# Performance work log

Hardware: AMD Instinct MI355X
Metric: run time of the kernel (lower is better)

## Reference

```python
import jax, jax.numpy as jnp
import numpy as np

E, S = 32768, 16
H, D_IN, EDGE_IN = 128, 128, 16
N_SRC, N_DST = 20000, 5000
HEADS, LAYERS, NUM_CLASS = 8, 2, 10
DH = H // HEADS


def _layer_norm(x, g, b, eps=1e-5):
    mu = jnp.mean(x, axis=-1, keepdims=True)
    var = jnp.mean((x - mu) ** 2, axis=-1, keepdims=True)
    return (x - mu) * jax.lax.rsqrt(var + eps) * g + b


def _encoder(e, e_mask, Wqkv, bqkv, Wo, bo, ln1_g, ln1_b, W1, b1, W2, b2, ln2_g, ln2_b):
    # e: [E,S,H]; e_mask: [E,S], True = padding. Post-norm encoder (PyTorch default).
    neg = jnp.float32(-1e9)
    for l in range(LAYERS):
        qkv = e @ Wqkv[l] + bqkv[l]                      # [E,S,3H]
        q, k, v = jnp.split(qkv, 3, axis=-1)
        q = q.reshape(E, S, HEADS, DH)
        k = k.reshape(E, S, HEADS, DH)
        v = v.reshape(E, S, HEADS, DH)
        scores = jnp.einsum('eqhd,ekhd->ehqk', q, k) / np.float32(np.sqrt(DH))
        scores = jnp.where(e_mask[:, None, None, :], neg, scores)
        attn = jax.nn.softmax(scores, axis=-1)
        ctx = jnp.einsum('ehqk,ekhd->eqhd', attn, v).reshape(E, S, H)
        e = _layer_norm(e + (ctx @ Wo[l] + bo[l]), ln1_g[l], ln1_b[l])
        ff = jax.nn.relu(e @ W1[l] + b1[l]) @ W2[l] + b2[l]
        e = _layer_norm(e + ff, ln2_g[l], ln2_b[l])
    return e


def _forward(node_features, edge_features, seq_times, subg_norm,
             W_ein, b_ein, enc_Wqkv, enc_bqkv, enc_Wo, enc_bo, enc_ln1_g, enc_ln1_b,
             enc_W1, enc_b1, enc_W2, enc_b2, enc_ln2_g, enc_ln2_b,
             W_eout, b_eout, W_node, b_node, W_fc, b_fc,
             e_len, e_mask, src_ids, dst_ids, layer_nid):
    h = node_features                                             # [N_src, D_IN]
    self_h = h[layer_nid]                                         # [N_dst, D_IN]
    self_h_tmp = jnp.concatenate([self_h, jnp.zeros((N_DST, H), h.dtype)], axis=1) @ W_eout + b_eout
    # message_func: per-edge sequence -> embed -> transformer -> pool -> concat with src h
    e = jnp.concatenate([edge_features, seq_times[..., None]], axis=-1)  # [E,S,EDGE_IN]
    e = jax.nn.relu(e @ W_ein + b_ein)                                   # [E,S,H]
    e = _encoder(e, e_mask, enc_Wqkv, enc_bqkv, enc_Wo, enc_bo,
                 enc_ln1_g, enc_ln1_b, enc_W1, enc_b1, enc_W2, enc_b2, enc_ln2_g, enc_ln2_b)
    valid = (~e_mask).astype(e.dtype)[..., None]
    e = jnp.sum(e * valid, axis=1) / e_len.astype(e.dtype)[:, None]      # masked mean pool [E,H]
    m = jax.nn.relu(jnp.concatenate([h[src_ids], e], axis=1) @ W_eout + b_eout)  # [E,H]
    h_agg = jax.ops.segment_sum(m, dst_ids, num_segments=N_DST)          # ragged mailbox sum
    hh = (h_agg - self_h_tmp) * subg_norm                                # NodeUpdate (train branch)
    z = jax.nn.relu(jnp.concatenate([self_h, hh], axis=1) @ W_node + b_node)
    return z @ W_fc + b_fc                                               # [N_dst, NUM_CLASS]


def setup_inputs() -> dict:
    key = jax.random.key(0)
    ks = jax.random.split(key, 32)
    inp = {}
    inp['node_features'] = jax.random.normal(ks[0], (N_SRC, D_IN), jnp.float32)
    inp['edge_features'] = jax.random.normal(ks[1], (E, S, EDGE_IN - 1), jnp.float32)
    inp['seq_times'] = jax.random.uniform(ks[2], (E, S), jnp.float32)
    e_len = jax.random.randint(ks[3], (E,), 1, S + 1).astype(jnp.int32)
    inp['e_len'] = e_len
    inp['e_mask'] = jnp.arange(S, dtype=jnp.int32)[None, :] >= e_len[:, None]  # True = pad
    inp['src_ids'] = jax.random.randint(ks[4], (E,), 0, N_SRC).astype(jnp.int32)
    inp['dst_ids'] = jax.random.randint(ks[5], (E,), 0, N_DST).astype(jnp.int32)
    inp['layer_nid'] = jax.random.randint(ks[6], (N_DST,), 0, N_SRC).astype(jnp.int32)
    inp['subg_norm'] = jax.random.uniform(ks[7], (N_DST, 1), jnp.float32, minval=0.01, maxval=1.0)

    def lin(k, fi, fo):
        return jax.random.normal(k, (fi, fo), jnp.float32) / np.float32(np.sqrt(fi))

    inp['W_ein'] = lin(ks[8], EDGE_IN, H); inp['b_ein'] = jnp.zeros((H,), jnp.float32)
    inp['enc_Wqkv'] = jax.random.normal(ks[9], (LAYERS, H, 3 * H), jnp.float32) / np.float32(np.sqrt(H))
    inp['enc_bqkv'] = jnp.zeros((LAYERS, 3 * H), jnp.float32)
    inp['enc_Wo'] = jax.random.normal(ks[10], (LAYERS, H, H), jnp.float32) / np.float32(np.sqrt(H))
    inp['enc_bo'] = jnp.zeros((LAYERS, H), jnp.float32)
    inp['enc_ln1_g'] = jnp.ones((LAYERS, H), jnp.float32); inp['enc_ln1_b'] = jnp.zeros((LAYERS, H), jnp.float32)
    inp['enc_W1'] = jax.random.normal(ks[11], (LAYERS, H, H), jnp.float32) / np.float32(np.sqrt(H))
    inp['enc_b1'] = jnp.zeros((LAYERS, H), jnp.float32)
    inp['enc_W2'] = jax.random.normal(ks[12], (LAYERS, H, H), jnp.float32) / np.float32(np.sqrt(H))
    inp['enc_b2'] = jnp.zeros((LAYERS, H), jnp.float32)
    inp['enc_ln2_g'] = jnp.ones((LAYERS, H), jnp.float32); inp['enc_ln2_b'] = jnp.zeros((LAYERS, H), jnp.float32)
    inp['W_eout'] = lin(ks[13], D_IN + H, H); inp['b_eout'] = jnp.zeros((H,), jnp.float32)
    inp['W_node'] = lin(ks[14], D_IN + H, H); inp['b_node'] = jnp.zeros((H,), jnp.float32)
    inp['W_fc'] = lin(ks[15], H, NUM_CLASS); inp['b_fc'] = jnp.zeros((NUM_CLASS,), jnp.float32)
    return inp


def reference(node_features, edge_features, seq_times, e_len, e_mask, src_ids, dst_ids,
              layer_nid, subg_norm, W_ein, b_ein, enc_Wqkv, enc_bqkv, enc_Wo, enc_bo,
              enc_ln1_g, enc_ln1_b, enc_W1, enc_b1, enc_W2, enc_b2, enc_ln2_g, enc_ln2_b,
              W_eout, b_eout, W_node, b_node, W_fc, b_fc):
    return _forward(node_features, edge_features, seq_times, subg_norm,
                    W_ein, b_ein, enc_Wqkv, enc_bqkv, enc_Wo, enc_bo, enc_ln1_g, enc_ln1_b,
                    enc_W1, enc_b1, enc_W2, enc_b2, enc_ln2_g, enc_ln2_b,
                    W_eout, b_eout, W_node, b_node, W_fc, b_fc,
                    e_len, e_mask, src_ids, dst_ids, layer_nid)
```

## Files before the change

### kernel.cpp

```cpp
#include <hip/hip_runtime.h>
#include <hip/hip_bf16.h>

typedef __attribute__((ext_vector_type(8))) short bf16x8;
typedef __attribute__((ext_vector_type(4))) short s16x4;
typedef __attribute__((ext_vector_type(4))) float f32x4;

#define E_N      32768
#define N_DST_N  5000
#define NCLS     10

#define OFF_HAGG   0
#define OFF_POOL   2560000
#define OFF_WPACK  10948608

#define PK_QKV(l)  ((l) * 6144)
#define PK_WO(l)   (12288 + (l) * 2048)
#define PK_W1(l)   (16384 + (l) * 2048)
#define PK_W2(l)   (20480 + (l) * 2048)
#define PK_WEOUT   24576
#define PK_WEIN    28672

__device__ __forceinline__ unsigned short f2bf(float f) {
    __hip_bfloat16 h = __float2bfloat16(f);
    unsigned short u;
    __builtin_memcpy(&u, &h, 2);
    return u;
}
__device__ __forceinline__ unsigned int f2bf2(float lo, float hi) {
    __hip_bfloat162 h = __float22bfloat162_rn(make_float2(lo, hi));
    unsigned int u;
    __builtin_memcpy(&u, &h, 4);
    return u;
}

__global__ void pack_weights(const float* __restrict__ Wqkv,
                             const float* __restrict__ Wo,
                             const float* __restrict__ W1,
                             const float* __restrict__ W2,
                             const float* __restrict__ W_eout,
                             const float* __restrict__ W_ein,
                             unsigned short* __restrict__ wpack) {
    int gid = blockIdx.x * 256 + threadIdx.x;
    if (gid >= 233472) return;
    if (gid >= 229376) {
        int li = gid - 229376;
        int j = li & 7, lane = (li >> 3) & 63, t = li >> 9;
        int k = ((lane >> 4) << 3) + j;
        int n = t * 16 + (lane & 15);
        wpack[gid] = (k < 16) ? f2bf(W_ein[k * 128 + n]) : (unsigned short)0;
        return;
    }
    int id = gid;
    const float* src; int K, N, li;
    if (id < 98304)       { src = Wqkv + (id / 49152) * 49152; li = id % 49152; K = 128; N = 384; }
    else if (id < 131072) { id -= 98304;  src = Wo + (id / 16384) * 16384; li = id % 16384; K = 128; N = 128; }
    else if (id < 163840) { id -= 131072; src = W1 + (id / 16384) * 16384; li = id % 16384; K = 128; N = 128; }
    else if (id < 196608) { id -= 163840; src = W2 + (id / 16384) * 16384; li = id % 16384; K = 128; N = 128; }
    else                  { li = id - 196608; src = W_eout; K = 256; N = 128; }
    int j = li & 7, lane = (li >> 3) & 63, rest = li >> 9;
    int ks = K >> 5;
    int kk = rest % ks, t = rest / ks;
    int k = kk * 32 + ((lane >> 4) << 3) + j;
    int n = t * 16 + (lane & 15);
    wpack[gid] = f2bf(src[k * N + n]);
}

__device__ __forceinline__ void layer_norm_reg(
    float res[2][2][4],
    const float gcol[2], const float bcol[2],
    unsigned short (*a_bf)[136],
    float (*psum)[4], float (*psq)[4],
    int w, int c16, int row4)
{
    float sv[2][4], qv[2][4];
#pragma unroll
    for (int rt = 0; rt < 2; ++rt)
#pragma unroll
        for (int r = 0; r < 4; ++r) {
            float x0 = res[rt][0][r], x1 = res[rt][1][r];
            float s = x0 + x1;
            float q = x0 * x0 + x1 * x1;
#pragma unroll
            for (int d = 1; d < 16; d <<= 1) {
                s += __shfl_xor(s, d);
                q += __shfl_xor(q, d);
            }
            sv[rt][r] = s; qv[rt][r] = q;
        }
    if (c16 == 0) {
#pragma unroll
        for (int rt = 0; rt < 2; ++rt)
#pragma unroll
            for (int r = 0; r < 4; ++r) {
                int row = rt * 16 + row4 + r;
                psum[row][w] = sv[rt][r];
                psq[row][w]  = qv[rt][r];
            }
    }
    __syncthreads();
#pragma unroll
    for (int rt = 0; rt < 2; ++rt)
#pragma unroll
        for (int r = 0; r < 4; ++r) {
            int row = rt * 16 + row4 + r;
            float4 S = *(const float4*)&psum[row][0];
            float4 Q = *(const float4*)&psq[row][0];
            float sum = (S.x + S.y) + (S.z + S.w);
            float sq  = (Q.x + Q.y) + (Q.z + Q.w);
            float mu  = sum * (1.f / 128.f);
            float var = sq * (1.f / 128.f) - mu * mu;
            float inv = rsqrtf(var + 1e-5f);
#pragma unroll
            for (int ti = 0; ti < 2; ++ti) {
                float y = (res[rt][ti][r] - mu) * inv * gcol[ti] + bcol[ti];
                res[rt][ti][r] = y;
                a_bf[row][w * 32 + ti * 16 + c16] = f2bf(y);
            }
        }
}

__global__ __launch_bounds__(256) void edge_kernel(
    const float* __restrict__ edge_features,
    const float* __restrict__ seq_times,
    const int*   __restrict__ e_len,
    const float* __restrict__ b_ein,
    const float* __restrict__ bqkv,  const float* __restrict__ bo,
    const float* __restrict__ ln1_g, const float* __restrict__ ln1_b,
    const float* __restrict__ b1,    const float* __restrict__ b2,
    const float* __restrict__ ln2_g, const float* __restrict__ ln2_b,
    const unsigned short* __restrict__ wpack,
    unsigned short* __restrict__ pooled)
{
    __shared__ __align__(16) unsigned short a_bf[32][136];
    __shared__ __align__(16) unsigned short q_bf[32][136];
    __shared__ __align__(16) unsigned short k_bf[32][136];
    __shared__ __align__(16) union VX {
        unsigned short vT[2][128][24];
        unsigned short x_bf[32][40];
    } vx;
    __shared__ __align__(16) float psum[32][4];
    __shared__ __align__(16) float psq[32][4];

    const int tid  = threadIdx.x;
    const int e0   = blockIdx.x * 2;
    const int lane = tid & 63;
    const int w    = tid >> 6;
    const int c16  = lane & 15;
    const int g    = lane >> 4;
    const int row4 = g << 2;
    const int kblk = g << 3;
    const int len0 = e_len[e0];
    const int len1 = e_len[e0 + 1];
    const f32x4 z4 = {0.f, 0.f, 0.f, 0.f};

    float res[2][2][4];

    float lnG[2][2][2], lnB[2][2][2];
#pragma unroll
    for (int l = 0; l < 2; ++l)
#pragma unroll
        for (int ti = 0; ti < 2; ++ti) {
            int col = w * 32 + ti * 16 + c16;
            lnG[l][0][ti] = ln1_g[l * 128 + col];
            lnB[l][0][ti] = ln1_b[l * 128 + col];
            lnG[l][1][ti] = ln2_g[l * 128 + col];
            lnB[l][1][ti] = ln2_b[l * 128 + col];
        }

    for (int idx = tid; idx < 1024; idx += 256) {
        int r = idx >> 5, cc = idx & 31;
        int e = r >> 4, s = r & 15;
        float v = 0.f;
        if (cc < 15)       v = edge_features[(e0 + e) * 240 + s * 15 + cc];
        else if (cc == 15) v = seq_times[(e0 + e) * 16 + s];
        vx.x_bf[r][cc] = f2bf(v);
    }
    __syncthreads();

    const bf16x8* WP = (const bf16x8*)wpack;

    {
        bf16x8 axf[2];
#pragma unroll
        for (int rt = 0; rt < 2; ++rt)
            axf[rt] = *(const bf16x8*)&vx.x_bf[rt * 16 + c16][kblk];
#pragma unroll
        for (int ti = 0; ti < 2; ++ti) {
            bf16x8 bw = WP[PK_WEIN + (2 * w + ti) * 64 + lane];
            int col = (2 * w + ti) * 16 + c16;
            float bias = b_ein[col];
#pragma unroll
            for (int rt = 0; rt < 2; ++rt) {
                f32x4 acc = __builtin_amdgcn_mfma_f32_16x16x32_bf16(axf[rt], bw, z4, 0, 0, 0);
#pragma unroll
                for (int r = 0; r < 4; ++r) {
                    float v = fmaxf(acc[r] + bias, 0.f);
                    res[rt][ti][r] = v;
                    a_bf[rt * 16 + row4 + r][col] = f2bf(v);
                }
            }
        }
    }
    __syncthreads();

    for (int l = 0; l < 2; ++l) {
        {
            bf16x8 af[2][4];
#pragma unroll
            for (int rt = 0; rt < 2; ++rt)
#pragma unroll
                for (int kk = 0; kk < 4; ++kk)
                    af[rt][kk] = *(const bf16x8*)&a_bf[rt * 16 + c16][kk * 32 + kblk];
            const bf16x8* B = WP + PK_QKV(l);
#pragma unroll
            for (int seg = 0; seg < 3; ++seg) {
#pragma unroll
                for (int ti = 0; ti < 2; ++ti) {
                    bf16x8 bq[4];
#pragma unroll
                    for (int kk = 0; kk < 4; ++kk)
                        bq[kk] = B[((seg * 8 + 2 * w + ti) * 4 + kk) * 64 + lane];
                    int col = (2 * w + ti) * 16 + c16;
                    float bias = bqkv[l * 384 + seg * 128 + col];
#pragma unroll
                    for (int rt = 0; rt < 2; ++rt) {
                        f32x4 acc = z4;
#pragma unroll
                        for (int kk = 0; kk < 4; ++kk)
                            acc = __builtin_amdgcn_mfma_f32_16x16x32_bf16(
                                af[rt][kk], bq[kk], acc, 0, 0, 0);
                        if (seg == 0) {
#pragma unroll
                            for (int r = 0; r < 4; ++r)
                                q_bf[rt * 16 + row4 + r][col] = f2bf(acc[r] + bias);
                        } else if (seg == 1) {
#pragma unroll
                            for (int r = 0; r < 4; ++r)
                                k_bf[rt * 16 + row4 + r][col] = f2bf(acc[r] + bias);
                        } else {
                            union { unsigned int u[2]; s16x4 v; } pk;
                            pk.u[0] = f2bf2(acc[0] + bias, acc[1] + bias);
                            pk.u[1] = f2bf2(acc[2] + bias, acc[3] + bias);
                            *(s16x4*)&vx.vT[rt][col][row4] = pk.v;
                        }
                    }
                }
            }
        }
        __syncthreads();

#pragma unroll
        for (int i = 0; i < 4; ++i) {
            int pp = w * 4 + i;
            int e  = pp >> 3;
            int hb = (pp & 7) * 16;
            int er = e * 16;
            int len = e ? len1 : len0;
            bf16x8 kf = {0,0,0,0,0,0,0,0};
            bf16x8 qf = {0,0,0,0,0,0,0,0};
            bf16x8 vf = {0,0,0,0,0,0,0,0};
            if (lane < 32) {
                kf = *(const bf16x8*)&k_bf[er + c16][hb + kblk];
                qf = *(const bf16x8*)&q_bf[er + c16][hb + kblk];
                vf = *(const bf16x8*)&vx.vT[e][hb + c16][kblk];
            }
            f32x4 st = __builtin_amdgcn_mfma_f32_16x16x32_bf16(kf, qf, z4, 0, 0, 0);
            float sv[4]; float mx = -1e30f;
#pragma unroll
            for (int r = 0; r < 4; ++r) {
                sv[r] = st[r] * 0.25f;
                if (4 * g + r < len) mx = fmaxf(mx, sv[r]);
            }
            mx = fmaxf(mx, __shfl_xor(mx, 16));
            mx = fmaxf(mx, __shfl_xor(mx, 32));
            float p[4]; float sum = 0.f;
#pragma unroll
            for (int r = 0; r < 4; ++r) {
                float pe = (4 * g + r < len) ? __expf(sv[r] - mx) : 0.f;
                p[r] = pe; sum += pe;
            }
            sum += __shfl_xor(sum, 16);
            sum += __shfl_xor(sum, 32);
            float inv = __fdividef(1.f, sum);
            unsigned int own0 = f2bf2(p[0] * inv, p[1] * inv);
            unsigned int own1 = f2bf2(p[2] * inv, p[3] * inv);
            unsigned int t0a = (unsigned int)__shfl((int)own0, (lane + 16) & 63);
            unsigned int t1a = (unsigned int)__shfl((int)own1, (lane + 16) & 63);
            unsigned int t0b = (unsigned int)__shfl((int)own0, (lane + 32) & 63);
            unsigned int t1b = (unsigned int)__shfl((int)own1, (lane + 32) & 63);
            union { unsigned int u[4]; bf16x8 v; } pb;
            if (g == 0)      { pb.u[0] = own0; pb.u[1] = own1; pb.u[2] = t0a; pb.u[3] = t1a; }
            else if (g == 1) { pb.u[0] = t0a;  pb.u[1] = t1a;  pb.u[2] = t0b; pb.u[3] = t1b; }
            else             { pb.u[0] = 0; pb.u[1] = 0; pb.u[2] = 0; pb.u[3] = 0; }
            f32x4 ct = __builtin_amdgcn_mfma_f32_16x16x32_bf16(vf, pb.v, z4, 0, 0, 0);
            union { unsigned int u[2]; s16x4 v; } cpk;
            cpk.u[0] = f2bf2(ct[0], ct[1]);
            cpk.u[1] = f2bf2(ct[2], ct[3]);
            *(s16x4*)&a_bf[er + c16][hb + 4 * g] = cpk.v;
        }
        __syncthreads();

        {
            bf16x8 af[2][4];
#pragma unroll
            for (int rt = 0; rt < 2; ++rt)
#pragma unroll
                for (int kk = 0; kk < 4; ++kk)
                    af[rt][kk] = *(const bf16x8*)&a_bf[rt * 16 + c16][kk * 32 + kblk];
            const bf16x8* B = WP + PK_WO(l);
#pragma unroll
            for (int ti = 0; ti < 2; ++ti) {
                bf16x8 bw[4];
#pragma unroll
                for (int kk = 0; kk < 4; ++kk)
                    bw[kk] = B[((2 * w + ti) * 4 + kk) * 64 + lane];
                int col = (2 * w + ti) * 16 + c16;
                float bias = bo[l * 128 + col];
#pragma unroll
                for (int rt = 0; rt < 2; ++rt) {
                    f32x4 acc = z4;
#pragma unroll
                    for (int kk = 0; kk < 4; ++kk)
                        acc = __builtin_amdgcn_mfma_f32_16x16x32_bf16(
                            af[rt][kk], bw[kk], acc, 0, 0, 0);
#pragma unroll
                    for (int r = 0; r < 4; ++r)
                        res[rt][ti][r] += acc[r] + bias;
                }
            }
        }
        layer_norm_reg(res, lnG[l][0], lnB[l][0], a_bf, psum, psq, w, c16, row4);
        __syncthreads();

        {
            bf16x8 af[2][4];
#pragma unroll
            for (int rt = 0; rt < 2; ++rt)
#pragma unroll
                for (int kk = 0; kk < 4; ++kk)
                    af[rt][kk] = *(const bf16x8*)&a_bf[rt * 16 + c16][kk * 32 + kblk];
            const bf16x8* B = WP + PK_W1(l);
#pragma unroll
            for (int ti = 0; ti < 2; ++ti) {
                bf16x8 bw[4];
#pragma unroll
                for (int kk = 0; kk < 4; ++kk)
                    bw[kk] = B[((2 * w + ti) * 4 + kk) * 64 + lane];
                int col = (2 * w + ti) * 16 + c16;
                float bias = b1[l * 128 + col];
#pragma unroll
                for (int rt = 0; rt < 2; ++rt) {
                    f32x4 acc = z4;
#pragma unroll
                    for (int kk = 0; kk < 4; ++kk)
                        acc = __builtin_amdgcn_mfma_f32_16x16x32_bf16(
                            af[rt][kk], bw[kk], acc, 0, 0, 0);
#pragma unroll
                    for (int r = 0; r < 4; ++r)
                        q_bf[rt * 16 + row4 + r][col] =
                            f2bf(fmaxf(acc[r] + bias, 0.f));
                }
            }
        }
        __syncthreads();

        {
            bf16x8 af[2][4];
#pragma unroll
            for (int rt = 0; rt < 2; ++rt)
#pragma unroll
                for (int kk = 0; kk < 4; ++kk)
                    af[rt][kk] = *(const bf16x8*)&q_bf[rt * 16 + c16][kk * 32 + kblk];
            const bf16x8* B = WP + PK_W2(l);
#pragma unroll
            for (int ti = 0; ti < 2; ++ti) {
                bf16x8 bw[4];
#pragma unroll
                for (int kk = 0; kk < 4; ++kk)
                    bw[kk] = B[((2 * w + ti) * 4 + kk) * 64 + lane];
                int col = (2 * w + ti) * 16 + c16;
                float bias = b2[l * 128 + col];
#pragma unroll
                for (int rt = 0; rt < 2; ++rt) {
                    f32x4 acc = z4;
#pragma unroll
                    for (int kk = 0; kk < 4; ++kk)
                        acc = __builtin_amdgcn_mfma_f32_16x16x32_bf16(
                            af[rt][kk], bw[kk], acc, 0, 0, 0);
#pragma unroll
                    for (int r = 0; r < 4; ++r)
                        res[rt][ti][r] += acc[r] + bias;
                }
            }
        }
        layer_norm_reg(res, lnG[l][1], lnB[l][1], a_bf, psum, psq, w, c16, row4);
        __syncthreads();
    }

#pragma unroll
    for (int rt = 0; rt < 2; ++rt) {
        int len = rt ? len1 : len0;
        float fln = (float)len;
#pragma unroll
        for (int ti = 0; ti < 2; ++ti) {
            float s = 0.f;
#pragma unroll
            for (int r = 0; r < 4; ++r)
                if (row4 + r < len) s += res[rt][ti][r];
            s += __shfl_xor(s, 16);
            s += __shfl_xor(s, 32);
            if (lane < 16)
                pooled[(e0 + rt) * 128 + w * 32 + ti * 16 + c16] = f2bf(s / fln);
        }
    }
}

__global__ __launch_bounds__(256) void edge_out_kernel(
    const float* __restrict__ node_features,
    const int* __restrict__ src_ids, const int* __restrict__ dst_ids,
    const unsigned short* __restrict__ pooled,
    const unsigned short* __restrict__ wpack,
    const float* __restrict__ b_eout,
    float* __restrict__ h_agg)
{
    __shared__ __align__(16) unsigned short a2[16][264];
    __shared__ int dst_s[16];
    const int tid = threadIdx.x, lane = tid & 63, w = tid >> 6;
    const int e0 = blockIdx.x * 16;

    {
        int r = tid >> 4, cm = tid & 15;
        int e = e0 + r;
        int src = src_ids[e];
#pragma unroll
        for (int m = 0; m < 8; ++m) {
            int col = cm + 16 * m;
            a2[r][col] = f2bf(node_features[src * 128 + col]);
        }
#pragma unroll
        for (int m = 0; m < 8; ++m) {
            int col = cm + 16 * m;
            a2[r][128 + col] = pooled[e * 128 + col];
        }
        if (tid < 16) dst_s[tid] = dst_ids[e0 + tid];
    }
    __syncthreads();

    const int c16 = lane & 15, row4 = (lane >> 4) << 2, kblk = (lane >> 4) << 3;
    bf16x8 af[8];
#pragma unroll
    for (int kk = 0; kk < 8; ++kk)
        af[kk] = *(const bf16x8*)&a2[c16][kk * 32 + kblk];
    const bf16x8* B = (const bf16x8*)wpack + PK_WEOUT;
#pragma unroll
    for (int ti = 0; ti < 2; ++ti) {
        int t = w * 2 + ti;
        f32x4 acc = {0.f, 0.f, 0.f, 0.f};
#pragma unroll
        for (int kk = 0; kk < 8; ++kk)
            acc = __builtin_amdgcn_mfma_f32_16x16x32_bf16(
                af[kk], B[(t * 8 + kk) * 64 + lane], acc, 0, 0, 0);
        int col = t * 16 + c16;
        float bias = b_eout[col];
#pragma unroll
        for (int r = 0; r < 4; ++r) {
            int row = row4 + r;
            float v = fmaxf(acc[r] + bias, 0.f);
            atomicAdd(&h_agg[dst_s[row] * 128 + col], v);
        }
    }
}

__global__ __launch_bounds__(128) void node_kernel(
    const float* __restrict__ node_features,
    const int*   __restrict__ layer_nid,
    const float* __restrict__ subg_norm,
    const float* __restrict__ h_agg,
    const float* __restrict__ W_eout, const float* __restrict__ b_eout,
    const float* __restrict__ W_node, const float* __restrict__ b_node,
    const float* __restrict__ W_fc,   const float* __restrict__ b_fc,
    float* __restrict__ out)
{
    __shared__ float sh[128];
    __shared__ float hh[128];
    __shared__ float z[128];

    const int n   = blockIdx.x;
    const int tid = threadIdx.x;
    const int nid = layer_nid[n];
    const float norm = subg_norm[n];

    sh[tid] = node_features[nid * 128 + tid];
    __syncthreads();

    float acc = 0.f;
#pragma unroll 4
    for (int k = 0; k < 128; ++k)
        acc = fmaf(sh[k], W_eout[k * 128 + tid], acc);
    acc += b_eout[tid];
    hh[tid] = (h_agg[n * 128 + tid] - acc) * norm;
    __syncthreads();

    float za = 0.f;
#pragma unroll 4
    for (int k = 0; k < 128; ++k)
        za = fmaf(sh[k], W_node[k * 128 + tid], za);
#pragma unroll 4
    for (int k = 0; k < 128; ++k)
        za = fmaf(hh[k], W_node[(128 + k) * 128 + tid], za);
    za += b_node[tid];
    z[tid] = fmaxf(za, 0.f);
    __syncthreads();

    if (tid < NCLS) {
        float o = 0.f;
#pragma unroll 4
        for (int k = 0; k < 128; ++k)
            o = fmaf(z[k], W_fc[k * NCLS + tid], o);
        out[n * NCLS + tid] = o + b_fc[tid];
    }
}


extern "C" void kernel_launch(void* const* d_in, const int* in_sizes, int n_in,
                              void* d_out, int out_size, void* d_ws, size_t ws_size,
                              hipStream_t stream) {
    const float* node_features = (const float*)d_in[0];
    const float* edge_features = (const float*)d_in[1];
    const float* seq_times     = (const float*)d_in[2];
    const int*   e_len         = (const int*)d_in[3];
    const int*   src_ids       = (const int*)d_in[5];
    const int*   dst_ids       = (const int*)d_in[6];
    const int*   layer_nid     = (const int*)d_in[7];
    const float* subg_norm     = (const float*)d_in[8];
    const float* W_ein  = (const float*)d_in[9];
    const float* b_ein  = (const float*)d_in[10];
    const float* Wqkv   = (const float*)d_in[11];
    const float* bqkv   = (const float*)d_in[12];
    const float* Wo     = (const float*)d_in[13];
    const float* bo     = (const float*)d_in[14];
    const float* ln1_g  = (const float*)d_in[15];
    const float* ln1_b  = (const float*)d_in[16];
    const float* W1     = (const float*)d_in[17];
    const float* b1     = (const float*)d_in[18];
    const float* W2     = (const float*)d_in[19];
    const float* b2     = (const float*)d_in[20];
    const float* ln2_g  = (const float*)d_in[21];
    const float* ln2_b  = (const float*)d_in[22];
    const float* W_eout = (const float*)d_in[23];
    const float* b_eout = (const float*)d_in[24];
    const float* W_node = (const float*)d_in[25];
    const float* b_node = (const float*)d_in[26];
    const float* W_fc   = (const float*)d_in[27];
    const float* b_fc   = (const float*)d_in[28];

    float*          h_agg  = (float*)((char*)d_ws + OFF_HAGG);
    unsigned short* pooled = (unsigned short*)((char*)d_ws + OFF_POOL);
    unsigned short* wpack  = (unsigned short*)((char*)d_ws + OFF_WPACK);

    pack_weights<<<912, 256, 0, stream>>>(Wqkv, Wo, W1, W2, W_eout, W_ein, wpack);
    hipMemsetAsync(h_agg, 0, (size_t)N_DST_N * 128 * sizeof(float), stream);

    edge_kernel<<<E_N / 2, 256, 0, stream>>>(
        edge_features, seq_times, e_len,
        b_ein, bqkv, bo, ln1_g, ln1_b, b1, b2, ln2_g, ln2_b,
        wpack, pooled);

    edge_out_kernel<<<E_N / 16, 256, 0, stream>>>(
        node_features, src_ids, dst_ids, pooled, wpack, b_eout, h_agg);

    node_kernel<<<N_DST_N, 128, 0, stream>>>(
        node_features, layer_nid, subg_norm, h_agg,
        W_eout, b_eout, W_node, b_node, W_fc, b_fc, (float*)d_out);
}
```

Baseline: 813.7 us.

## Process four edges per block with eight waves, each owning one column tile

The edge transformer kernel now handles 4 edges (64 rows) per 512-thread block instead of 2 edges per 256-thread block. Each of the 8 waves owns one 16-column tile of every GEMM and loads its weight fragments once for all four row tiles. This halves the number of blocks and the per-edge weight fetches. The FFN intermediate moves into a separate shared buffer unioned with vT, and layer-norm gains/biases are now read per call instead of being preloaded. In exchange, shared memory per block roughly doubles and each block is larger, which may lower occupancy.

Result: slower. 1.384 ms (+70.1%).

```diff
diff --git a/kernel.cpp b/kernel.cpp
--- a/kernel.cpp
+++ b/kernel.cpp
@@ -66,20 +66,18 @@
 }
 
 __device__ __forceinline__ void layer_norm_reg(
-    float res[2][2][4],
-    const float gcol[2], const float bcol[2],
+    float res[4][4], float gv, float bv,
     unsigned short (*a_bf)[136],
-    float (*psum)[4], float (*psq)[4],
-    int w, int c16, int row4)
+    float (*psum)[8], float (*psq)[8],
+    int w, int c16, int row4, int col)
 {
-    float sv[2][4], qv[2][4];
-#pragma unroll
-    for (int rt = 0; rt < 2; ++rt)
+    float sv[4][4], qv[4][4];
+#pragma unroll
+    for (int rt = 0; rt < 4; ++rt)
 #pragma unroll
         for (int r = 0; r < 4; ++r) {
-            float x0 = res[rt][0][r], x1 = res[rt][1][r];
-            float s = x0 + x1;
-            float q = x0 * x0 + x1 * x1;
+            float x = res[rt][r];
+            float s = x, q = x * x;
 #pragma unroll
             for (int d = 1; d < 16; d <<= 1) {
                 s += __shfl_xor(s, d);
@@ -89,7 +87,7 @@
         }
     if (c16 == 0) {
 #pragma unroll
-        for (int rt = 0; rt < 2; ++rt)
+        for (int rt = 0; rt < 4; ++rt)
 #pragma unroll
             for (int r = 0; r < 4; ++r) {
                 int row = rt * 16 + row4 + r;
@@ -99,27 +97,26 @@
     }
     __syncthreads();
 #pragma unroll
-    for (int rt = 0; rt < 2; ++rt)
+    for (int rt = 0; rt < 4; ++rt)
 #pragma unroll
         for (int r = 0; r < 4; ++r) {
             int row = rt * 16 + row4 + r;
-            float4 S = *(const float4*)&psum[row][0];
-            float4 Q = *(const float4*)&psq[row][0];
-            float sum = (S.x + S.y) + (S.z + S.w);
-            float sq  = (Q.x + Q.y) + (Q.z + Q.w);
+            float4 S0 = *(const float4*)&psum[row][0];
+            float4 S1 = *(const float4*)&psum[row][4];
+            float4 Q0 = *(const float4*)&psq[row][0];
+            float4 Q1 = *(const float4*)&psq[row][4];
+            float sum = ((S0.x + S0.y) + (S0.z + S0.w)) + ((S1.x + S1.y) + (S1.z + S1.w));
+            float sq  = ((Q0.x + Q0.y) + (Q0.z + Q0.w)) + ((Q1.x + Q1.y) + (Q1.z + Q1.w));
             float mu  = sum * (1.f / 128.f);
             float var = sq * (1.f / 128.f) - mu * mu;
             float inv = rsqrtf(var + 1e-5f);
-#pragma unroll
-            for (int ti = 0; ti < 2; ++ti) {
-                float y = (res[rt][ti][r] - mu) * inv * gcol[ti] + bcol[ti];
-                res[rt][ti][r] = y;
-                a_bf[row][w * 32 + ti * 16 + c16] = f2bf(y);
-            }
-        }
-}
-
-__global__ __launch_bounds__(256) void edge_kernel(
+            float y = (res[rt][r] - mu) * inv * gv + bv;
+            res[rt][r] = y;
+            a_bf[row][col] = f2bf(y);
+        }
+}
+
+__global__ __launch_bounds__(512) void edge_kernel(
     const float* __restrict__ edge_features,
     const float* __restrict__ seq_times,
     const int*   __restrict__ e_len,
@@ -131,43 +128,35 @@
     const unsigned short* __restrict__ wpack,
     unsigned short* __restrict__ pooled)
 {
-    __shared__ __align__(16) unsigned short a_bf[32][136];
-    __shared__ __align__(16) unsigned short q_bf[32][136];
-    __shared__ __align__(16) unsigned short k_bf[32][136];
+    __shared__ __align__(16) unsigned short a_bf[64][136];
+    __shared__ __align__(16) unsigned short q_bf[64][136];
+    __shared__ __align__(16) unsigned short k_bf[64][136];
     __shared__ __align__(16) union VX {
-        unsigned short vT[2][128][24];
-        unsigned short x_bf[32][40];
+        unsigned short vT[4][128][24];
+        unsigned short x_bf[64][40];
+        unsigned short ff[64][136];
     } vx;
-    __shared__ __align__(16) float psum[32][4];
-    __shared__ __align__(16) float psq[32][4];
+    __shared__ __align__(16) float psum[64][8];
+    __shared__ __align__(16) float psq[64][8];
 
     const int tid  = threadIdx.x;
-    const int e0   = blockIdx.x * 2;
+    const int e0   = blockIdx.x * 4;
     const int lane = tid & 63;
     const int w    = tid >> 6;
     const int c16  = lane & 15;
     const int g    = lane >> 4;
     const int row4 = g << 2;
     const int kblk = g << 3;
+    const int col  = w * 16 + c16;
     const int len0 = e_len[e0];
     const int len1 = e_len[e0 + 1];
+    const int len2 = e_len[e0 + 2];
+    const int len3 = e_len[e0 + 3];
     const f32x4 z4 = {0.f, 0.f, 0.f, 0.f};
 
-    float res[2][2][4];
-
-    float lnG[2][2][2], lnB[2][2][2];
-#pragma unroll
-    for (int l = 0; l < 2; ++l)
-#pragma unroll
-        for (int ti = 0; ti < 2; ++ti) {
-            int col = w * 32 + ti * 16 + c16;
-            lnG[l][0][ti] = ln1_g[l * 128 + col];
-            lnB[l][0][ti] = ln1_b[l * 128 + col];
-            lnG[l][1][ti] = ln2_g[l * 128 + col];
-            lnB[l][1][ti] = ln2_b[l * 128 + col];
-        }
-
-    for (int idx = tid; idx < 1024; idx += 256) {
+    float res[4][4];
+
+    for (int idx = tid; idx < 2048; idx += 512) {
         int r = idx >> 5, cc = idx & 31;
         int e = r >> 4, s = r & 15;
         float v = 0.f;
@@ -180,24 +169,17 @@
     const bf16x8* WP = (const bf16x8*)wpack;
 
     {
-        bf16x8 axf[2];
-#pragma unroll
-        for (int rt = 0; rt < 2; ++rt)
-            axf[rt] = *(const bf16x8*)&vx.x_bf[rt * 16 + c16][kblk];
-#pragma unroll
-        for (int ti = 0; ti < 2; ++ti) {
-            bf16x8 bw = WP[PK_WEIN + (2 * w + ti) * 64 + lane];
-            int col = (2 * w + ti) * 16 + c16;
-            float bias = b_ein[col];
-#pragma unroll
-            for (int rt = 0; rt < 2; ++rt) {
-                f32x4 acc = __builtin_amdgcn_mfma_f32_16x16x32_bf16(axf[rt], bw, z4, 0, 0, 0);
-#pragma unroll
-                for (int r = 0; r < 4; ++r) {
-                    float v = fmaxf(acc[r] + bias, 0.f);
-                    res[rt][ti][r] = v;
-                    a_bf[rt * 16 + row4 + r][col] = f2bf(v);
-                }
+        bf16x8 bw = WP[PK_WEIN + w * 64 + lane];
+        float bias = b_ein[col];
+#pragma unroll
+        for (int rt = 0; rt < 4; ++rt) {
+            bf16x8 axf = *(const bf16x8*)&vx.x_bf[rt * 16 + c16][kblk];
+            f32x4 acc = __builtin_amdgcn_mfma_f32_16x16x32_bf16(axf, bw, z4, 0, 0, 0);
+#pragma unroll
+            for (int r = 0; r < 4; ++r) {
+                float v = fmaxf(acc[r] + bias, 0.f);
+                res[rt][r] = v;
+                a_bf[rt * 16 + row4 + r][col] = f2bf(v);
             }
         }
     }
@@ -205,43 +187,48 @@
 
     for (int l = 0; l < 2; ++l) {
         {
-            bf16x8 af[2][4];
-#pragma unroll
-            for (int rt = 0; rt < 2; ++rt)
-#pragma unroll
-                for (int kk = 0; kk < 4; ++kk)
-                    af[rt][kk] = *(const bf16x8*)&a_bf[rt * 16 + c16][kk * 32 + kblk];
-            const bf16x8* B = WP + PK_QKV(l);
-#pragma unroll
-            for (int seg = 0; seg < 3; ++seg) {
-#pragma unroll
-                for (int ti = 0; ti < 2; ++ti) {
+#pragma unroll
+            for (int half = 0; half < 2; ++half) {
+                bf16x8 af[2][4];
+#pragma unroll
+                for (int r2 = 0; r2 < 2; ++r2)
+#pragma unroll
+                    for (int kk = 0; kk < 4; ++kk)
+                        af[r2][kk] = *(const bf16x8*)
+                            &a_bf[(half * 2 + r2) * 16 + c16][kk * 32 + kblk];
+                const bf16x8* B = WP + PK_QKV(l);
+#pragma unroll
+                for (int j = 0; j < 3; ++j) {
+                    int t = w * 3 + j;
                     bf16x8 bq[4];
 #pragma unroll
                     for (int kk = 0; kk < 4; ++kk)
-                        bq[kk] = B[((seg * 8 + 2 * w + ti) * 4 + kk) * 64 + lane];
-                    int col = (2 * w + ti) * 16 + c16;
-                    float bias = bqkv[l * 384 + seg * 128 + col];
-#pragma unroll
-                    for (int rt = 0; rt < 2; ++rt) {
+                        bq[kk] = B[(t * 4 + kk) * 64 + lane];
+                    int seg = t >> 3;
+                    int tc  = t & 7;
+                    int oc  = tc * 16 + c16;
+                    float bias = bqkv[l * 384 + seg * 128 + oc];
+#pragma unroll
+                    for (int r2 = 0; r2 < 2; ++r2) {
+                        int rt = half * 2 + r2;
                         f32x4 acc = z4;
 #pragma unroll
                         for (int kk = 0; kk < 4; ++kk)
                             acc = __builtin_amdgcn_mfma_f32_16x16x32_bf16(
-                                af[rt][kk], bq[kk], acc, 0, 0, 0);
+                                af[r2][kk], bq[kk], acc, 0, 0, 0);
                         if (seg == 0) {
 #pragma unroll
                             for (int r = 0; r < 4; ++r)
-                                q_bf[rt * 16 + row4 + r][col] = f2bf(acc[r] + bias);
+                                q_bf[rt * 16 + row4 + r][oc] = f2bf(acc[r] + bias);
                         } else if (seg == 1) {
 #pragma unroll
                             for (int r = 0; r < 4; ++r)
-                                k_bf[rt * 16 + row4 + r][col] = f2bf(acc[r] + bias);
+                                k_bf[rt * 16 + row4 + r][oc] = f2bf(acc[r] + bias);
                         } else {
                             union { unsigned int u[2]; s16x4 v; } pk;
                             pk.u[0] = f2bf2(acc[0] + bias, acc[1] + bias);
                             pk.u[1] = f2bf2(acc[2] + bias, acc[3] + bias);
-                            *(s16x4*)&vx.vT[rt][col][row4] = pk.v;
+                            *(s16x4*)&vx.vT[rt][oc][row4] = pk.v;
                         }
                     }
                 }
@@ -255,7 +242,7 @@
             int e  = pp >> 3;
             int hb = (pp & 7) * 16;
             int er = e * 16;
-            int len = e ? len1 : len0;
+            int len = (e == 0) ? len0 : ((e == 1) ? len1 : ((e == 2) ? len2 : len3));
             bf16x8 kf = {0,0,0,0,0,0,0,0};
             bf16x8 qf = {0,0,0,0,0,0,0,0};
             bf16x8 vf = {0,0,0,0,0,0,0,0};
@@ -301,63 +288,66 @@
         __syncthreads();
 
         {
-            bf16x8 af[2][4];
-#pragma unroll
-            for (int rt = 0; rt < 2; ++rt)
-#pragma unroll
-                for (int kk = 0; kk < 4; ++kk)
-                    af[rt][kk] = *(const bf16x8*)&a_bf[rt * 16 + c16][kk * 32 + kblk];
             const bf16x8* B = WP + PK_WO(l);
-#pragma unroll
-            for (int ti = 0; ti < 2; ++ti) {
-                bf16x8 bw[4];
-#pragma unroll
-                for (int kk = 0; kk < 4; ++kk)
-                    bw[kk] = B[((2 * w + ti) * 4 + kk) * 64 + lane];
-                int col = (2 * w + ti) * 16 + c16;
-                float bias = bo[l * 128 + col];
-#pragma unroll
-                for (int rt = 0; rt < 2; ++rt) {
+            bf16x8 bw[4];
+#pragma unroll
+            for (int kk = 0; kk < 4; ++kk)
+                bw[kk] = B[(w * 4 + kk) * 64 + lane];
+            float bias = bo[l * 128 + col];
+#pragma unroll
+            for (int half = 0; half < 2; ++half) {
+                bf16x8 af[2][4];
+#pragma unroll
+                for (int r2 = 0; r2 < 2; ++r2)
+#pragma unroll
+                    for (int kk = 0; kk < 4; ++kk)
+                        af[r2][kk] = *(const bf16x8*)
+                            &a_bf[(half * 2 + r2) * 16 + c16][kk * 32 + kblk];
+#pragma unroll
+                for (int r2 = 0; r2 < 2; ++r2) {
+                    int rt = half * 2 + r2;
                     f32x4 acc = z4;
 #pragma unroll
                     for (int kk = 0; kk < 4; ++kk)
                         acc = __builtin_amdgcn_mfma_f32_16x16x32_bf16(
-                            af[rt][kk], bw[kk], acc, 0, 0, 0);
+                            af[r2][kk], bw[kk], acc, 0, 0, 0);
 #pragma unroll
                     for (int r = 0; r < 4; ++r)
-                        res[rt][ti][r] += acc[r] + bias;
+                        res[rt][r] += acc[r] + bias;
                 }
             }
         }
-        layer_norm_reg(res, lnG[l][0], lnB[l][0], a_bf, psum, psq, w, c16, row4);
+        layer_norm_reg(res, ln1_g[l * 128 + col], ln1_b[l * 128 + col],
+                       a_bf, psum, psq, w, c16, row4, col);
         __syncthreads();
 
         {
-            bf16x8 af[2][4];
-#pragma unroll
-            for (int rt = 0; rt < 2; ++rt)
-#pragma unroll
-                for (int kk = 0; kk < 4; ++kk)
-                    af[rt][kk] = *(const bf16x8*)&a_bf[rt * 16 + c16][kk * 32 + kblk];
             const bf16x8* B = WP + PK_W1(l);
-#pragma unroll
-            for (int ti = 0; ti < 2; ++ti) {
-                bf16x8 bw[4];
-#pragma unroll
-                for (int kk = 0; kk < 4; ++kk)
-                    bw[kk] = B[((2 * w + ti) * 4 + kk) * 64 + lane];
-                int col = (2 * w + ti) * 16 + c16;
-                float bias = b1[l * 128 + col];
-#pragma unroll
-                for (int rt = 0; rt < 2; ++rt) {
+            bf16x8 bw[4];
+#pragma unroll
+            for (int kk = 0; kk < 4; ++kk)
+                bw[kk] = B[(w * 4 + kk) * 64 + lane];
+            float bias = b1[l * 128 + col];
+#pragma unroll
+            for (int half = 0; half < 2; ++half) {
+                bf16x8 af[2][4];
+#pragma unroll
+                for (int r2 = 0; r2 < 2; ++r2)
+#pragma unroll
+                    for (int kk = 0; kk < 4; ++kk)
+                        af[r2][kk] = *(const bf16x8*)
+                            &a_bf[(half * 2 + r2) * 16 + c16][kk * 32 + kblk];
+#pragma unroll
+                for (int r2 = 0; r2 < 2; ++r2) {
+                    int rt = half * 2 + r2;
                     f32x4 acc = z4;
 #pragma unroll
                     for (int kk = 0; kk < 4; ++kk)
                         acc = __builtin_amdgcn_mfma_f32_16x16x32_bf16(
-                            af[rt][kk], bw[kk], acc, 0, 0, 0);
+                            af[r2][kk], bw[kk], acc, 0, 0, 0);
 #pragma unroll
                     for (int r = 0; r < 4; ++r)
-                        q_bf[rt * 16 + row4 + r][col] =
+                        vx.ff[rt * 16 + row4 + r][col] =
                             f2bf(fmaxf(acc[r] + bias, 0.f));
                 }
             }
@@ -365,53 +355,52 @@
         __syncthreads();
 
         {
-            bf16x8 af[2][4];
-#pragma unroll
-            for (int rt = 0; rt < 2; ++rt)
-#pragma unroll
-                for (int kk = 0; kk < 4; ++kk)
-                    af[rt][kk] = *(const bf16x8*)&q_bf[rt * 16 + c16][kk * 32 + kblk];
             const bf16x8* B = WP + PK_W2(l);
-#pragma unroll
-            for (int ti = 0; ti < 2; ++ti) {
-                bf16x8 bw[4];
-#pragma unroll
-                for (int kk = 0; kk < 4; ++kk)
-                    bw[kk] = B[((2 * w + ti) * 4 + kk) * 64 + lane];
-                int col = (2 * w + ti) * 16 + c16;
-                float bias = b2[l * 128 + col];
-#pragma unroll
-                for (int rt = 0; rt < 2; ++rt) {
+            bf16x8 bw[4];
+#pragma unroll
+            for (int kk = 0; kk < 4; ++kk)
+                bw[kk] = B[(w * 4 + kk) * 64 + lane];
+            float bias = b2[l * 128 + col];
+#pragma unroll
+            for (int half = 0; half < 2; ++half) {
+                bf16x8 af[2][4];
+#pragma unroll
+                for (int r2 = 0; r2 < 2; ++r2)
+#pragma unroll
+                    for (int kk = 0; kk < 4; ++kk)
+                        af[r2][kk] = *(const bf16x8*)
+                            &vx.ff[(half * 2 + r2) * 16 + c16][kk * 32 + kblk];
+#pragma unroll
+                for (int r2 = 0; r2 < 2; ++r2) {
+                    int rt = half * 2 + r2;
                     f32x4 acc = z4;
 #pragma unroll
                     for (int kk = 0; kk < 4; ++kk)
                         acc = __builtin_amdgcn_mfma_f32_16x16x32_bf16(
-                            af[rt][kk], bw[kk], acc, 0, 0, 0);
+                            af[r2][kk], bw[kk], acc, 0, 0, 0);
 #pragma unroll
                     for (int r = 0; r < 4; ++r)
-                        res[rt][ti][r] += acc[r] + bias;
+                        res[rt][r] += acc[r] + bias;
                 }
             }
         }
-        layer_norm_reg(res, lnG[l][1], lnB[l][1], a_bf, psum, psq, w, c16, row4);
+        layer_norm_reg(res, ln2_g[l * 128 + col], ln2_b[l * 128 + col],
+                       a_bf, psum, psq, w, c16, row4, col);
         __syncthreads();
     }
 
 #pragma unroll
-    for (int rt = 0; rt < 2; ++rt) {
-        int len = rt ? len1 : len0;
+    for (int rt = 0; rt < 4; ++rt) {
+        int len = (rt == 0) ? len0 : ((rt == 1) ? len1 : ((rt == 2) ? len2 : len3));
         float fln = (float)len;
-#pragma unroll
-        for (int ti = 0; ti < 2; ++ti) {
-            float s = 0.f;
-#pragma unroll
-            for (int r = 0; r < 4; ++r)
-                if (row4 + r < len) s += res[rt][ti][r];
-            s += __shfl_xor(s, 16);
-            s += __shfl_xor(s, 32);
-            if (lane < 16)
-                pooled[(e0 + rt) * 128 + w * 32 + ti * 16 + c16] = f2bf(s / fln);
-        }
+        float s = 0.f;
+#pragma unroll
+        for (int r = 0; r < 4; ++r)
+            if (row4 + r < len) s += res[rt][r];
+        s += __shfl_xor(s, 16);
+        s += __shfl_xor(s, 32);
+        if (lane < 16)
+            pooled[(e0 + rt) * 128 + col] = f2bf(s / fln);
     }
 }
 
@@ -561,7 +550,7 @@
     pack_weights<<<912, 256, 0, stream>>>(Wqkv, Wo, W1, W2, W_eout, W_ein, wpack);
     hipMemsetAsync(h_agg, 0, (size_t)N_DST_N * 128 * sizeof(float), stream);
 
-    edge_kernel<<<E_N / 2, 256, 0, stream>>>(
+    edge_kernel<<<E_N / 4, 512, 0, stream>>>(
         edge_features, seq_times, e_len,
         b_ein, bqkv, bo, ln1_g, ln1_b, b1, b2, ln2_g, ln2_b,
         wpack, pooled);
```
